# Kernel optimization log

Hardware: AMD Instinct MI355X
Metric: run time of the kernel (lower is better)

Reference implementation:

```python
import jax, jax.numpy as jnp
import numpy as np


def setup_inputs() -> dict:
    key = jax.random.key(0)
    ks = jax.random.split(key, 6)
    shapes = [
        (2048, 128, 64),   # large: shape[1] > 64
        (2048, 32, 32),    # small -> fused bucket
        (2048, 64, 64),    # small (== 64 is not > 64) -> fused bucket
        (2048, 16, 48),    # small -> fused bucket
        (2048, 200, 32),   # large: shape[1] > 64
        (2048, 8, 8),      # small -> fused bucket
    ]
    inp = {f"x{i}": jax.random.normal(ks[i], s, dtype=jnp.float32) for i, s in enumerate(shapes)}
    inp["dim"] = 1  # dim[0] in the original module: reduce over the middle (list-length) axis
    return inp


def reference(x0, x1, x2, x3, x4, x5, dim):
    # ComboSumModule: outputs[i] = input_list[i].sum(dim[0]).
    # The size-bucketing (shape[1]>64 or shape[2]>64) only changes kernel
    # fusion, not the math, so each tensor is reduced independently.
    xs = (x0, x1, x2, x3, x4, x5)
    return tuple(jnp.sum(x, axis=dim) for x in xs)
```

## Files before the change

kernel.cpp:

```cpp
#include <hip/hip_runtime.h>


__device__ __forceinline__ float4 f4add(float4 a, float4 b) {
  return make_float4(a.x + b.x, a.y + b.y, a.z + b.z, a.w + b.w);
}

template <int M, int N, int CNT>
__device__ __forceinline__ float4 partial(const float* __restrict__ xp,
                                          int group, int row_start, int lane) {
  constexpr int N4 = N / 4;
  const int u = group * 64 + lane;
  const int b = u / N4;
  const int n4 = u - b * N4;
  const float4* __restrict__ p =
      reinterpret_cast<const float4*>(xp) + (size_t)b * (M * N4) +
      (size_t)row_start * N4 + n4;

  float4 v[CNT];
#pragma unroll
  for (int i = 0; i < CNT; ++i) v[i] = p[(size_t)i * N4];

  float4 r = v[CNT - 1];
#pragma unroll
  for (int i = CNT - 2; i >= 0; --i) r = f4add(r, v[i]);
  return r;
}

template <int WPG>
__device__ __forceinline__ void combine(float4 r, float* __restrict__ out,
                                        int out_base4, int group, int wave,
                                        int lane, float4* lds) {
  if (WPG == 1) {
    reinterpret_cast<float4*>(out)[out_base4 + group * 64 + lane] = r;
    return;
  }
  lds[wave * 64 + lane] = r;
  __syncthreads();
  if ((wave & (WPG - 1)) == 0) {
    float4 s = lds[wave * 64 + lane];
#pragma unroll
    for (int j = 1; j < WPG; ++j) s = f4add(s, lds[(wave + j) * 64 + lane]);
    reinterpret_cast<float4*>(out)[out_base4 + group * 64 + lane] = s;
  }
}

__global__ __launch_bounds__(1024) void ComboSumModule_25314537242674_kernel(
    const float* __restrict__ x0, const float* __restrict__ x1,
    const float* __restrict__ x2, const float* __restrict__ x3,
    const float* __restrict__ x4, const float* __restrict__ x5,
    float* __restrict__ out) {
  __shared__ float4 lds[16 * 64];
  const int lane = threadIdx.x & 63;
  const int wave = threadIdx.x >> 6;
  const int blk = blockIdx.x;

  if (blk < 256) {
    float4 r;
    if (wave < 8)
      r = partial<200, 32, 13>(x4, blk, 13 * wave, lane);
    else
      r = partial<200, 32, 12>(x4, blk, 104 + 12 * (wave - 8), lane);
    combine<16>(r, out, 106496, blk, wave, lane, lds);
  } else if (blk < 768) {
    float4 r = partial<128, 64, 8>(x0, blk - 256, 8 * wave, lane);
    combine<16>(r, out, 0, blk - 256, wave, lane, lds);
  } else if (blk < 1024) {
    const int g = (blk - 768) * 2 + (wave >> 3);
    float4 r = partial<64, 64, 8>(x2, g, 8 * (wave & 7), lane);
    combine<8>(r, out, 49152, g, wave, lane, lds);
  } else if (blk < 1088) {
    const int g = (blk - 1024) * 4 + (wave >> 2);
    float4 r = partial<32, 32, 8>(x1, g, 8 * (wave & 3), lane);
    combine<4>(r, out, 32768, g, wave, lane, lds);
  } else if (blk < 1136) {
    const int g = (blk - 1088) * 8 + (wave >> 1);
    float4 r = partial<16, 48, 8>(x3, g, 8 * (wave & 1), lane);
    combine<2>(r, out, 81920, g, wave, lane, lds);
  } else {
    const int g = (blk - 1136) * 16 + wave;
    float4 r = partial<8, 8, 8>(x5, g, 0, lane);
    combine<1>(r, out, 122880, g, wave, lane, lds);
  }
}

extern "C" void kernel_launch(void* const* d_in, const int* in_sizes, int n_in,
                              void* d_out, int out_size, void* d_ws, size_t ws_size,
                              hipStream_t stream) {
  const float* x0 = (const float*)d_in[0];
  const float* x1 = (const float*)d_in[1];
  const float* x2 = (const float*)d_in[2];
  const float* x3 = (const float*)d_in[3];
  const float* x4 = (const float*)d_in[4];
  const float* x5 = (const float*)d_in[5];
  float* out = (float*)d_out;

  ComboSumModule_25314537242674_kernel<<<1140, 1024, 0, stream>>>(
      x0, x1, x2, x3, x4, x5, out);
}
```

Measured before the change: 177.1 us.

## Restructure reduction to per-wave tasks with double-buffered loads and shuffle combine

Measured after the change: 185.1 us. +4.5%, slower.

```diff
diff --git a/kernel.cpp b/kernel.cpp
--- a/kernel.cpp
+++ b/kernel.cpp
@@ -5,87 +5,126 @@
   return make_float4(a.x + b.x, a.y + b.y, a.z + b.z, a.w + b.w);
 }
 
-template <int M, int N, int CNT>
-__device__ __forceinline__ float4 partial(const float* __restrict__ xp,
-                                          int group, int row_start, int lane) {
-  constexpr int N4 = N / 4;
-  const int u = group * 64 + lane;
-  const int b = u / N4;
-  const int n4 = u - b * N4;
-  const float4* __restrict__ p =
-      reinterpret_cast<const float4*>(xp) + (size_t)b * (M * N4) +
-      (size_t)row_start * N4 + n4;
-
-  float4 v[CNT];
+template <int STRIDE4, int B>
+__device__ __forceinline__ void load_batch(float4 (&v)[B],
+                                           const float4* __restrict__ q) {
 #pragma unroll
-  for (int i = 0; i < CNT; ++i) v[i] = p[(size_t)i * N4];
-
-  float4 r = v[CNT - 1];
-#pragma unroll
-  for (int i = CNT - 2; i >= 0; --i) r = f4add(r, v[i]);
-  return r;
+  for (int i = 0; i < B; ++i) v[i] = q[(size_t)i * STRIDE4];
 }
 
-template <int WPG>
-__device__ __forceinline__ void combine(float4 r, float* __restrict__ out,
-                                        int out_base4, int group, int wave,
-                                        int lane, float4* lds) {
-  if (WPG == 1) {
-    reinterpret_cast<float4*>(out)[out_base4 + group * 64 + lane] = r;
-    return;
-  }
-  lds[wave * 64 + lane] = r;
-  __syncthreads();
-  if ((wave & (WPG - 1)) == 0) {
-    float4 s = lds[wave * 64 + lane];
+template <int B>
+__device__ __forceinline__ void add_batch(const float4 (&v)[B], float4& a0,
+                                          float4& a1, float4& a2, float4& a3) {
 #pragma unroll
-    for (int j = 1; j < WPG; ++j) s = f4add(s, lds[(wave + j) * 64 + lane]);
-    reinterpret_cast<float4*>(out)[out_base4 + group * 64 + lane] = s;
+  for (int i = 0; i < B; ++i) {
+    if ((i & 3) == 0) a0 = f4add(a0, v[i]);
+    else if ((i & 3) == 1) a1 = f4add(a1, v[i]);
+    else if ((i & 3) == 2) a2 = f4add(a2, v[i]);
+    else a3 = f4add(a3, v[i]);
   }
 }
 
-__global__ __launch_bounds__(1024) void ComboSumModule_25314537242674_kernel(
+template <int ROWS, int STRIDE4>
+__device__ __forceinline__ float4 col_sum(const float4* __restrict__ p) {
+  constexpr int B = (ROWS >= 8) ? 8 : ROWS;
+  constexpr int NB = ROWS / B;
+  constexpr int TAIL = ROWS - NB * B;
+
+  float4 va[B], vb[B];
+  float4 a0 = make_float4(0.f, 0.f, 0.f, 0.f);
+  float4 a1 = a0, a2 = a0, a3 = a0;
+
+  load_batch<STRIDE4>(va, p);
+  __builtin_amdgcn_sched_barrier(0);
+
+#pragma unroll
+  for (int k = 1; k < NB; ++k) {
+    const float4* q = p + (size_t)(k * B) * STRIDE4;
+    if (k & 1) {
+      load_batch<STRIDE4>(vb, q);
+      __builtin_amdgcn_sched_barrier(0);
+      add_batch(va, a0, a1, a2, a3);
+    } else {
+      load_batch<STRIDE4>(va, q);
+      __builtin_amdgcn_sched_barrier(0);
+      add_batch(vb, a0, a1, a2, a3);
+    }
+    __builtin_amdgcn_sched_barrier(0);
+  }
+
+  if constexpr (TAIL > 0) {
+    float4 vt[TAIL];
+    load_batch<STRIDE4>(vt, p + (size_t)(NB * B) * STRIDE4);
+    __builtin_amdgcn_sched_barrier(0);
+    if constexpr (((NB - 1) & 1) != 0) add_batch(vb, a0, a1, a2, a3);
+    else add_batch(va, a0, a1, a2, a3);
+    add_batch(vt, a0, a1, a2, a3);
+  } else {
+    if constexpr (((NB - 1) & 1) != 0) add_batch(vb, a0, a1, a2, a3);
+    else add_batch(va, a0, a1, a2, a3);
+  }
+  return f4add(f4add(a0, a1), f4add(a2, a3));
+}
+
+template <int M, int N, int SPLIT>
+__device__ __forceinline__ void tensor_sum(const float* __restrict__ xp,
+                                           float4* __restrict__ out4,
+                                           int task, int lane) {
+  constexpr int N4 = N / 4;
+  constexpr int UN = 64 / SPLIT;
+  constexpr int ROWS = M / SPLIT;
+  const int ul = lane & (UN - 1);
+  const int part = lane / UN;
+  const int u = task * UN + ul;
+  const int b = u / N4;
+  const int n4 = u - b * N4;
+  const float4* p = reinterpret_cast<const float4*>(xp) +
+                    (size_t)b * (M * N4) + (size_t)(part * ROWS) * N4 + n4;
+
+  float4 r = col_sum<ROWS, N4>(p);
+
+  if constexpr (SPLIT == 4) {
+    r.x += __shfl_xor(r.x, 16);
+    r.y += __shfl_xor(r.y, 16);
+    r.z += __shfl_xor(r.z, 16);
+    r.w += __shfl_xor(r.w, 16);
+  }
+  if constexpr (SPLIT >= 2) {
+    r.x += __shfl_xor(r.x, 32);
+    r.y += __shfl_xor(r.y, 32);
+    r.z += __shfl_xor(r.z, 32);
+    r.w += __shfl_xor(r.w, 32);
+  }
+  if (part == 0) out4[u] = r;
+}
+
+__global__ __launch_bounds__(256, 4) void ComboSumModule_25314537242674_kernel(
     const float* __restrict__ x0, const float* __restrict__ x1,
     const float* __restrict__ x2, const float* __restrict__ x3,
     const float* __restrict__ x4, const float* __restrict__ x5,
     float* __restrict__ out) {
-  __shared__ float4 lds[16 * 64];
   const int lane = threadIdx.x & 63;
-  const int wave = threadIdx.x >> 6;
-  const int blk = blockIdx.x;
+  const int wid = (blockIdx.x << 2) | (threadIdx.x >> 6);
+  float4* out4 = reinterpret_cast<float4*>(out);
 
-  if (blk < 256) {
-    float4 r;
-    if (wave < 8)
-      r = partial<200, 32, 13>(x4, blk, 13 * wave, lane);
-    else
-      r = partial<200, 32, 12>(x4, blk, 104 + 12 * (wave - 8), lane);
-    combine<16>(r, out, 106496, blk, wave, lane, lds);
-  } else if (blk < 768) {
-    float4 r = partial<128, 64, 8>(x0, blk - 256, 8 * wave, lane);
-    combine<16>(r, out, 0, blk - 256, wave, lane, lds);
-  } else if (blk < 1024) {
-    const int g = (blk - 768) * 2 + (wave >> 3);
-    float4 r = partial<64, 64, 8>(x2, g, 8 * (wave & 7), lane);
-    combine<8>(r, out, 49152, g, wave, lane, lds);
-  } else if (blk < 1088) {
-    const int g = (blk - 1024) * 4 + (wave >> 2);
-    float4 r = partial<32, 32, 8>(x1, g, 8 * (wave & 3), lane);
-    combine<4>(r, out, 32768, g, wave, lane, lds);
-  } else if (blk < 1136) {
-    const int g = (blk - 1088) * 8 + (wave >> 1);
-    float4 r = partial<16, 48, 8>(x3, g, 8 * (wave & 1), lane);
-    combine<2>(r, out, 81920, g, wave, lane, lds);
+  if (wid < 1024) {
+    tensor_sum<128, 64, 2>(x0, out4 + 0, wid, lane);
+  } else if (wid < 2048) {
+    tensor_sum<200, 32, 4>(x4, out4 + 106496, wid - 1024, lane);
+  } else if (wid < 2560) {
+    tensor_sum<64, 64, 1>(x2, out4 + 49152, wid - 2048, lane);
+  } else if (wid < 2816) {
+    tensor_sum<32, 32, 1>(x1, out4 + 32768, wid - 2560, lane);
+  } else if (wid < 3200) {
+    tensor_sum<16, 48, 1>(x3, out4 + 81920, wid - 2816, lane);
   } else {
-    const int g = (blk - 1136) * 16 + wave;
-    float4 r = partial<8, 8, 8>(x5, g, 0, lane);
-    combine<1>(r, out, 122880, g, wave, lane, lds);
+    tensor_sum<8, 8, 1>(x5, out4 + 122880, wid - 3200, lane);
   }
 }
 
 extern "C" void kernel_launch(void* const* d_in, const int* in_sizes, int n_in,
-                              void* d_out, int out_size, void* d_ws, size_t ws_size,
-                              hipStream_t stream) {
+                              void* d_out, int out_size, void* d_ws,
+                              size_t ws_size, hipStream_t stream) {
   const float* x0 = (const float*)d_in[0];
   const float* x1 = (const float*)d_in[1];
   const float* x2 = (const float*)d_in[2];
@@ -94,6 +133,6 @@
   const float* x5 = (const float*)d_in[5];
   float* out = (float*)d_out;
 
-  ComboSumModule_25314537242674_kernel<<<1140, 1024, 0, stream>>>(
-      x0, x1, x2, x3, x4, x5, out);
+  ComboSumModule_25314537242674_kernel<<<816, 256, 0, stream>>>(x0, x1, x2, x3,
+                                                                x4, x5, out);
 }
```

## Assign one wave per batch slab with shuffle reduction instead of LDS combine

Applied to the files above, without the earlier changes.

Result: slower. 185.6 us (+4.8%).

```diff
diff --git a/kernel.cpp b/kernel.cpp
--- a/kernel.cpp
+++ b/kernel.cpp
@@ -5,87 +5,121 @@
   return make_float4(a.x + b.x, a.y + b.y, a.z + b.z, a.w + b.w);
 }
 
-template <int M, int N, int CNT>
-__device__ __forceinline__ float4 partial(const float* __restrict__ xp,
-                                          int group, int row_start, int lane) {
-  constexpr int N4 = N / 4;
-  const int u = group * 64 + lane;
-  const int b = u / N4;
-  const int n4 = u - b * N4;
-  const float4* __restrict__ p =
-      reinterpret_cast<const float4*>(xp) + (size_t)b * (M * N4) +
-      (size_t)row_start * N4 + n4;
+__device__ __forceinline__ float4 f4zero() {
+  return make_float4(0.f, 0.f, 0.f, 0.f);
+}
 
-  float4 v[CNT];
-#pragma unroll
-  for (int i = 0; i < CNT; ++i) v[i] = p[(size_t)i * N4];
-
-  float4 r = v[CNT - 1];
-#pragma unroll
-  for (int i = CNT - 2; i >= 0; --i) r = f4add(r, v[i]);
+__device__ __forceinline__ float4 shfl_xor_add(float4 r, int off) {
+  r.x += __shfl_xor(r.x, off);
+  r.y += __shfl_xor(r.y, off);
+  r.z += __shfl_xor(r.z, off);
+  r.w += __shfl_xor(r.w, off);
   return r;
 }
 
-template <int WPG>
-__device__ __forceinline__ void combine(float4 r, float* __restrict__ out,
-                                        int out_base4, int group, int wave,
-                                        int lane, float4* lds) {
-  if (WPG == 1) {
-    reinterpret_cast<float4*>(out)[out_base4 + group * 64 + lane] = r;
-    return;
+template <int LOADS, int STRIDE4, int PIPE>
+__device__ __forceinline__ float4 roll_sum(const float4* __restrict__ p) {
+  constexpr int P = (LOADS < PIPE) ? LOADS : PIPE;
+  float4 v[P];
+  float4 a0 = f4zero(), a1 = f4zero();
+#pragma unroll
+  for (int i = 0; i < P; ++i) v[i] = p[(size_t)i * STRIDE4];
+#pragma unroll
+  for (int k = 0; k < LOADS - P; ++k) {
+    float4 t = v[k % P];
+    v[k % P] = p[(size_t)(k + P) * STRIDE4];
+    if (k & 1) a1 = f4add(a1, t);
+    else a0 = f4add(a0, t);
   }
-  lds[wave * 64 + lane] = r;
-  __syncthreads();
-  if ((wave & (WPG - 1)) == 0) {
-    float4 s = lds[wave * 64 + lane];
 #pragma unroll
-    for (int j = 1; j < WPG; ++j) s = f4add(s, lds[(wave + j) * 64 + lane]);
-    reinterpret_cast<float4*>(out)[out_base4 + group * 64 + lane] = s;
+  for (int k = LOADS - P; k < LOADS; ++k) {
+    if (k & 1) a1 = f4add(a1, v[k % P]);
+    else a0 = f4add(a0, v[k % P]);
+  }
+  return f4add(a0, a1);
+}
+
+template <int M, int N4>
+__device__ __forceinline__ void slab_sum(const float* __restrict__ xp,
+                                         float4* __restrict__ outp, int b,
+                                         int lane) {
+  constexpr int L = M * N4 / 64;
+  const float4* p =
+      reinterpret_cast<const float4*>(xp) + (size_t)b * (M * N4) + lane;
+  float4 r = roll_sum<L, 64, 8>(p);
+#pragma unroll
+  for (int off = N4; off < 64; off <<= 1) r = shfl_xor_add(r, off);
+  if (lane < N4) outp[(size_t)b * N4 + lane] = r;
+}
+
+__device__ __forceinline__ void x1_quad(const float* __restrict__ xp,
+                                        float4* __restrict__ outp, int w,
+                                        int lane) {
+  const int b0 = w << 2;
+  const float4* p =
+      reinterpret_cast<const float4*>(xp) + (size_t)b0 * 256 + lane;
+  float4 v[8];
+  float4 acc[4] = {f4zero(), f4zero(), f4zero(), f4zero()};
+#pragma unroll
+  for (int i = 0; i < 8; ++i) v[i] = p[(size_t)i * 64];
+#pragma unroll
+  for (int k = 0; k < 8; ++k) {
+    float4 t = v[k];
+    v[k] = p[(size_t)(k + 8) * 64];
+    acc[k >> 2] = f4add(acc[k >> 2], t);
+  }
+#pragma unroll
+  for (int k = 8; k < 16; ++k) acc[k >> 2] = f4add(acc[k >> 2], v[k - 8]);
+#pragma unroll
+  for (int j = 0; j < 4; ++j) {
+    float4 r = acc[j];
+    r = shfl_xor_add(r, 8);
+    r = shfl_xor_add(r, 16);
+    r = shfl_xor_add(r, 32);
+    if (lane < 8) outp[(size_t)(b0 + j) * 8 + lane] = r;
   }
 }
 
-__global__ __launch_bounds__(1024) void ComboSumModule_25314537242674_kernel(
+template <int M, int N4>
+__device__ __forceinline__ void col_walk(const float* __restrict__ xp,
+                                         float4* __restrict__ outp, int task,
+                                         int lane) {
+  const int u = task * 64 + lane;
+  const int b = u / N4;
+  const int n4 = u - b * N4;
+  const float4* p =
+      reinterpret_cast<const float4*>(xp) + (size_t)b * (M * N4) + n4;
+  outp[u] = roll_sum<M, N4, 8>(p);
+}
+
+__global__ __launch_bounds__(256, 8) void ComboSumModule_25314537242674_kernel(
     const float* __restrict__ x0, const float* __restrict__ x1,
     const float* __restrict__ x2, const float* __restrict__ x3,
     const float* __restrict__ x4, const float* __restrict__ x5,
     float* __restrict__ out) {
-  __shared__ float4 lds[16 * 64];
   const int lane = threadIdx.x & 63;
   const int wave = threadIdx.x >> 6;
   const int blk = blockIdx.x;
+  float4* out4 = reinterpret_cast<float4*>(out);
 
-  if (blk < 256) {
-    float4 r;
-    if (wave < 8)
-      r = partial<200, 32, 13>(x4, blk, 13 * wave, lane);
-    else
-      r = partial<200, 32, 12>(x4, blk, 104 + 12 * (wave - 8), lane);
-    combine<16>(r, out, 106496, blk, wave, lane, lds);
-  } else if (blk < 768) {
-    float4 r = partial<128, 64, 8>(x0, blk - 256, 8 * wave, lane);
-    combine<16>(r, out, 0, blk - 256, wave, lane, lds);
+  if (blk < 512) {
+    slab_sum<128, 16>(x0, out4 + 0, (blk << 2) | wave, lane);
   } else if (blk < 1024) {
-    const int g = (blk - 768) * 2 + (wave >> 3);
-    float4 r = partial<64, 64, 8>(x2, g, 8 * (wave & 7), lane);
-    combine<8>(r, out, 49152, g, wave, lane, lds);
-  } else if (blk < 1088) {
-    const int g = (blk - 1024) * 4 + (wave >> 2);
-    float4 r = partial<32, 32, 8>(x1, g, 8 * (wave & 3), lane);
-    combine<4>(r, out, 32768, g, wave, lane, lds);
-  } else if (blk < 1136) {
-    const int g = (blk - 1088) * 8 + (wave >> 1);
-    float4 r = partial<16, 48, 8>(x3, g, 8 * (wave & 1), lane);
-    combine<2>(r, out, 81920, g, wave, lane, lds);
+    slab_sum<200, 8>(x4, out4 + 106496, ((blk - 512) << 2) | wave, lane);
+  } else if (blk < 1536) {
+    slab_sum<64, 16>(x2, out4 + 49152, ((blk - 1024) << 2) | wave, lane);
+  } else if (blk < 1664) {
+    x1_quad(x1, out4 + 32768, ((blk - 1536) << 2) | wave, lane);
+  } else if (blk < 1760) {
+    col_walk<16, 12>(x3, out4 + 81920, ((blk - 1664) << 2) | wave, lane);
   } else {
-    const int g = (blk - 1136) * 16 + wave;
-    float4 r = partial<8, 8, 8>(x5, g, 0, lane);
-    combine<1>(r, out, 122880, g, wave, lane, lds);
+    col_walk<8, 2>(x5, out4 + 122880, ((blk - 1760) << 2) | wave, lane);
   }
 }
 
 extern "C" void kernel_launch(void* const* d_in, const int* in_sizes, int n_in,
-                              void* d_out, int out_size, void* d_ws, size_t ws_size,
-                              hipStream_t stream) {
+                              void* d_out, int out_size, void* d_ws,
+                              size_t ws_size, hipStream_t stream) {
   const float* x0 = (const float*)d_in[0];
   const float* x1 = (const float*)d_in[1];
   const float* x2 = (const float*)d_in[2];
@@ -94,6 +128,7 @@
   const float* x5 = (const float*)d_in[5];
   float* out = (float*)d_out;
 
-  ComboSumModule_25314537242674_kernel<<<1140, 1024, 0, stream>>>(
-      x0, x1, x2, x3, x4, x5, out);
+  ComboSumModule_25314537242674_kernel<<<1776, 256, 0, stream>>>(x0, x1, x2,
+                                                                 x3, x4, x5,
+                                                                 out);
 }
```
